# Kernel optimization log

Hardware: AMD Instinct MI355X
Metric: run time of the kernel (lower is better)

Reference implementation:

```python
import jax, jax.numpy as jnp
import numpy as np

A, NA, D_OBS, B = 16, 8, 64, 128  # agents, actions, obs dim, graphs
DZ = D_OBS + NA  # obs_z_input_dim = 72


def _mlp(x, W1, b1, W2, b2):
    # Linear -> leaky_relu(0.01) -> Linear, torch Linear convention (y = x @ W.T + b)
    return jax.nn.leaky_relu(x @ W1.T + b1) @ W2.T + b2


def setup_inputs() -> dict:
    key = jax.random.key(0)
    ks = iter(jax.random.split(key, 40))
    p = {}
    p["obs"] = jax.random.normal(next(ks), (B * A, D_OBS), jnp.float32)
    p["policies"] = jax.random.uniform(next(ks), (B * A, NA), jnp.float32)
    p["actions"] = jax.random.uniform(next(ks), (B * A, NA), jnp.float32)

    def mk(name, inp, out):
        p[name + "_w"] = jax.random.normal(next(ks), (out, inp), jnp.float32) / np.sqrt(inp).astype(np.float32)
        p[name + "_b"] = jax.random.normal(next(ks), (out,), jnp.float32) * 0.01

    mk("kw1", D_OBS, 64); mk("kw2", 64, 64)   # key_weight layers
    mk("qw1", D_OBS, 64); mk("qw2", 64, 64)   # query_weight layers
    mk("ko1", DZ, 64);    mk("ko2", 64, 64)   # key_obsz layers
    mk("qo1", DZ, 64);    mk("qo2", 64, 64)   # query_obsz layers
    mk("av1", DZ, 64);    mk("av2", 64, 64)   # attention_value_obsz layers
    mk("fv1", 128, 64);   mk("fv2", 64, 8)    # final_value layers
    return p


def reference(obs, policies, actions,
              kw1_w, kw1_b, kw2_w, kw2_b, qw1_w, qw1_b, qw2_w, qw2_b,
              ko1_w, ko1_b, ko2_w, ko2_b, qo1_w, qo1_b, qo2_w, qo2_b,
              av1_w, av1_b, av2_w, av2_b, fv1_w, fv1_b, fv2_w, fv2_b):
    d_k_w = jnp.sqrt(jnp.float32(kw2_w.shape[0]))
    d_k_o = jnp.sqrt(jnp.float32(ko2_w.shape[0]))
    Bn = obs.shape[0] // A
    obs_b = obs.reshape(Bn, A, -1)                      # [B,A,Dobs]
    pi = policies.reshape(Bn, A, NA)
    act = actions.reshape(Bn, A, NA)

    # --- DGL update_all on the fully-connected (with self-loop) per-batch graph ---
    key_z = _mlp(obs_b, kw1_w, kw1_b, kw2_w, kw2_b)     # [B,A,dk]
    query_z = _mlp(obs_b, qw1_w, qw1_b, qw2_w, qw2_b)
    score = jnp.einsum('bjd,bid->bij', key_z, query_z)  # src key j -> dst query i
    w = jax.nn.sigmoid(score / d_k_w)[..., None]        # [B,A,A,1], mailbox gate
    z = w * act[:, None] + (1.0 - w) * pi[:, None]      # [B,A(i),A(j),NA]
    weight_z = w.reshape(Bn * A, A, 1)

    # obs_z[b,i,j] = cat(obs[b,j], z[b,i,j])
    obs_rep = jnp.broadcast_to(obs_b[:, None], (Bn, A, A, obs_b.shape[-1]))
    obs_z = jnp.concatenate([obs_rep, z], axis=-1)      # [B,A,A,DZ]

    diag = jnp.arange(A)
    src = obs_z[:, diag, diag]                          # source_obs_z_: [B,A,DZ] (j==i entry)

    key_o = _mlp(src, ko1_w, ko1_b, ko2_w, ko2_b)       # broadcast over j
    query_o = _mlp(obs_z, qo1_w, qo1_b, qo2_w, qo2_b)   # [B,A,A,dk]
    score_o = jnp.einsum('bid,bijd->bij', key_o, query_o)
    weights_o = jax.nn.softmax(jnp.exp(jnp.clip(score_o / d_k_o, -5.0, 5.0)), axis=-1)  # [B,A,A]

    # obs_z_pi[b,i,j,k] = op[b,j] if k==j else obs_z[b,i,k], op = cat(obs, pi)
    op = jnp.concatenate([obs_b, pi], axis=-1)          # [B,A,DZ]
    m = jnp.eye(A, dtype=obs.dtype)[None, None, :, :, None]          # (j,k) mask
    obs_z_pi = obs_z[:, :, None] * (1.0 - m) + op[:, None, None] * m  # [B,A,A,A,DZ]

    attn_src = _mlp(src, av1_w, av1_b, av2_w, av2_b)                  # [B,A,O]
    attn_other = _mlp(obs_z_pi, av1_w, av1_b, av2_w, av2_b)           # [B,A,A,A,O]

    w_exp = weights_o[:, None, :, :, None]              # [b,i,j,k,1] = weights_o[b,j,k]
    mixed = jnp.mean(attn_other * w_exp, axis=-2)       # mean over k -> [B,A,A,O]
    src_rep = jnp.broadcast_to(attn_src[:, None], mixed.shape)
    node_features = jnp.concatenate([src_rep, mixed], axis=-1)        # [B,A,A,2O]
    value = _mlp(node_features, fv1_w, fv1_b, fv2_w, fv2_b)           # [B,A,A,8]

    weights_obsz = jnp.broadcast_to(w_exp, (Bn, A, A, A, 1))
    return value, weight_z, weights_obsz
```

## Files before the change

kernel.cpp:

```cpp
#include <hip/hip_runtime.h>

#define A_ 16
#define NA_ 8
#define DOBS_ 64

typedef _Float16 f16;
typedef f16 h2 __attribute__((ext_vector_type(2)));
typedef f16 v8h __attribute__((ext_vector_type(8)));
typedef float v4f __attribute__((ext_vector_type(4)));

__device__ __forceinline__ float fdot2f(h2 a, h2 b, float c) {
  return __builtin_amdgcn_fdot2(a, b, c, false);
}
__device__ __forceinline__ float lrelu(float x) { return x > 0.f ? x : 0.01f * x; }

struct P {
  const float *obs, *pol, *act;
  const float *kw1w, *kw1b, *kw2w, *kw2b, *qw1w, *qw1b, *qw2w, *qw2b;
  const float *ko1w, *ko1b, *ko2w, *ko2b, *qo1w, *qo1b, *qo2w, *qo2b;
  const float *av1w, *av1b, *av2w, *av2b, *fv1w, *fv1b, *fv2w, *fv2b;
  float *out0, *out1, *out2;
};

#define OBSH 0
#define OBSL 1152
#define X1Ho 2304
#define X1Lo 3456
#define X2Ho 4608
#define X2Lo 5760
#define EHO  6912
#define FLT  7168
#define F_PI   0
#define F_ACT  128
#define F_WSIG 256
#define F_WO   512
#define F_C0   768
#define F_S2   784
#define F_S3G  1872
#define F_WZK  2960
#define F_WZQ  3472
#define F_B    3984
#define WKW1  15648
#define WQW1  20256
#define WKW2  24864
#define WQW2  29472
#define WKO1H 34080
#define WKO1L 38688
#define WKO2H 43296
#define WKO2L 47904
#define WQO1H 52512
#define WQO1L 57120
#define WQO2H 61728
#define WQO2L 66336
#define AV1H  15648
#define AV2H  21792
#define BACKB1 26400
#define SLA   26656
#define SLB   70944
#define AOSRC 77088
#define APTO  78240
#define FV1H  34080
#define FV2PW 42784
#define BACKB2 43296
#define LDS_F16 79776

__device__ __forceinline__ v4f gemm_plain(const f16* Xh, const f16* W, float bv, int nt, int lane) {
  const int m = lane & 15, q = lane >> 4;
  v4f acc = {bv, bv, bv, bv};
  const v8h a0 = *(const v8h*)(Xh + m * 72 + q * 8);
  const v8h a1 = *(const v8h*)(Xh + m * 72 + 32 + q * 8);
  const f16* wr = W + (nt * 16 + m) * 72 + q * 8;
  acc = __builtin_amdgcn_mfma_f32_16x16x32_f16(a0, *(const v8h*)wr, acc, 0, 0, 0);
  acc = __builtin_amdgcn_mfma_f32_16x16x32_f16(a1, *(const v8h*)(wr + 32), acc, 0, 0, 0);
  return acc;
}

__device__ __forceinline__ v4f gemm_tile(const f16* Xh, const f16* Xl,
                                         const f16* Wh, const f16* Wl,
                                         float bv, int nt, int lane) {
  const int m = lane & 15, q = lane >> 4;
  v4f acc = {bv, bv, bv, bv};
  const v8h ah0 = *(const v8h*)(Xh + m * 72 + q * 8);
  const v8h ah1 = *(const v8h*)(Xh + m * 72 + 32 + q * 8);
  const v8h al0 = *(const v8h*)(Xl + m * 72 + q * 8);
  const v8h al1 = *(const v8h*)(Xl + m * 72 + 32 + q * 8);
  const f16* wr = Wh + (nt * 16 + m) * 72 + q * 8;
  const v8h bh0 = *(const v8h*)(wr);
  const v8h bh1 = *(const v8h*)(wr + 32);
  const f16* wr2 = Wl + (nt * 16 + m) * 72 + q * 8;
  const v8h bl0 = *(const v8h*)(wr2);
  const v8h bl1 = *(const v8h*)(wr2 + 32);
  acc = __builtin_amdgcn_mfma_f32_16x16x32_f16(ah0, bh0, acc, 0, 0, 0);
  acc = __builtin_amdgcn_mfma_f32_16x16x32_f16(ah1, bh1, acc, 0, 0, 0);
  acc = __builtin_amdgcn_mfma_f32_16x16x32_f16(ah0, bl0, acc, 0, 0, 0);
  acc = __builtin_amdgcn_mfma_f32_16x16x32_f16(ah1, bl1, acc, 0, 0, 0);
  acc = __builtin_amdgcn_mfma_f32_16x16x32_f16(al0, bh0, acc, 0, 0, 0);
  acc = __builtin_amdgcn_mfma_f32_16x16x32_f16(al1, bh1, acc, 0, 0, 0);
  return acc;
}

__device__ __forceinline__ void writeX(f16* Xh, f16* Xl, v4f acc, int nt, int lane, bool relu) {
  const int m = lane & 15, q = lane >> 4;
#pragma unroll
  for (int reg = 0; reg < 4; reg++) {
    float y = acc[reg];
    if (relu) y = lrelu(y);
    const f16 yh = (f16)y;
    Xh[(q * 4 + reg) * 72 + nt * 16 + m] = yh;
    Xl[(q * 4 + reg) * 72 + nt * 16 + m] = (f16)(y - (float)yh);
  }
}

__device__ __forceinline__ void putP(f16* W, float4 v, int o, int rq) {
  h2* d = (h2*)(W + o * 72 + 4 * rq);
  d[0] = h2{(f16)v.x, (f16)v.y};
  d[1] = h2{(f16)v.z, (f16)v.w};
}

__device__ __forceinline__ void putW(f16* Wh, f16* Wl, float4 v, int o, int rq) {
  h2* dh = (h2*)(Wh + o * 72 + 4 * rq);
  h2* dl = (h2*)(Wl + o * 72 + 4 * rq);
  const f16 hx = (f16)v.x, hy = (f16)v.y, hz = (f16)v.z, hw = (f16)v.w;
  dh[0] = h2{hx, hy};
  dh[1] = h2{hz, hw};
  dl[0] = h2{(f16)(v.x - (float)hx), (f16)(v.y - (float)hy)};
  dl[1] = h2{(f16)(v.z - (float)hz), (f16)(v.w - (float)hw)};
}

__device__ __forceinline__ v8h bfrag(const f16* Wm, int stride, int nt, int ks, int lane) {
  const int n = lane & 15, q = lane >> 4;
  return *(const v8h*)(Wm + (nt * 16 + n) * stride + ks * 32 + q * 8);
}

__device__ __forceinline__ void av_mlp2(const f16* obsh, const f16* av1H, const f16* av2H,
                                        const float* av1b, const float* av2b,
                                        f16* Hbuf, v8h az, int lane, v4f acc2[4]) {
  const int m = lane & 15, q = lane >> 4;
  const v8h a0 = *(const v8h*)(obsh + m * 72 + q * 8);
  const v8h a1 = *(const v8h*)(obsh + m * 72 + 32 + q * 8);
#pragma unroll
  for (int nt = 0; nt < 4; nt++) {
    const float bv = av1b[nt * 16 + m];
    v4f acc = {bv, bv, bv, bv};
    acc = __builtin_amdgcn_mfma_f32_16x16x32_f16(a0, bfrag(av1H, 96, nt, 0, lane), acc, 0, 0, 0);
    acc = __builtin_amdgcn_mfma_f32_16x16x32_f16(a1, bfrag(av1H, 96, nt, 1, lane), acc, 0, 0, 0);
    acc = __builtin_amdgcn_mfma_f32_16x16x32_f16(az, bfrag(av1H, 96, nt, 2, lane), acc, 0, 0, 0);
#pragma unroll
    for (int reg = 0; reg < 4; reg++)
      Hbuf[(q * 4 + reg) * 72 + nt * 16 + m] = (f16)lrelu(acc[reg]);
  }
  const v8h h0 = *(const v8h*)(Hbuf + m * 72 + q * 8);
  const v8h h1 = *(const v8h*)(Hbuf + m * 72 + 32 + q * 8);
#pragma unroll
  for (int nt = 0; nt < 4; nt++) {
    const float bv = av2b[nt * 16 + m];
    v4f acc = {bv, bv, bv, bv};
    acc = __builtin_amdgcn_mfma_f32_16x16x32_f16(h0, bfrag(av2H, 72, nt, 0, lane), acc, 0, 0, 0);
    acc = __builtin_amdgcn_mfma_f32_16x16x32_f16(h1, bfrag(av2H, 72, nt, 1, lane), acc, 0, 0, 0);
    acc2[nt] = acc;
  }
}

__global__ __launch_bounds__(512) void critic_fused(P p) {
  extern __shared__ f16 SMB[];
  float* F = (float*)(SMB + FLT);
  const int tid = threadIdx.x;
  const int b = blockIdx.x >> 1, ihalf = blockIdx.x & 1;
  const int w = tid >> 6, lane = tid & 63;
  const int m = lane & 15, quad = lane >> 4;
  const int o = tid & 63, r8 = tid >> 6;

  const float2 Robs = ((const float2*)(p.obs + (size_t)b * 1024))[tid];
  float Rpa = 0.f;
  if (tid < 128) Rpa = p.pol[(size_t)b * 128 + tid];
  else if (tid < 256) Rpa = p.act[(size_t)b * 128 + tid - 128];
  const float Rwzko = p.ko1w[(tid >> 3) * 72 + 64 + (tid & 7)];
  const float Rwzqo = p.qo1w[(tid >> 3) * 72 + 64 + (tid & 7)];
  float4 Rkw1[2], Rqw1[2], Rkw2[2], Rqw2[2], Rko1[2], Rko2[2], Rqo1[2], Rqo2[2];
#pragma unroll
  for (int h = 0; h < 2; h++) {
    const int rq = r8 + 8 * h;
    Rkw1[h] = *(const float4*)(p.kw1w + o * 64 + 4 * rq);
    Rqw1[h] = *(const float4*)(p.qw1w + o * 64 + 4 * rq);
    Rkw2[h] = *(const float4*)(p.kw2w + o * 64 + 4 * rq);
    Rqw2[h] = *(const float4*)(p.qw2w + o * 64 + 4 * rq);
    Rko1[h] = *(const float4*)(p.ko1w + o * 72 + 4 * rq);
    Rko2[h] = *(const float4*)(p.ko2w + o * 64 + 4 * rq);
    Rqo1[h] = *(const float4*)(p.qo1w + o * 72 + 4 * rq);
    Rqo2[h].x = p.qo2w[(4 * rq + 0) * 64 + o];
    Rqo2[h].y = p.qo2w[(4 * rq + 1) * 64 + o];
    Rqo2[h].z = p.qo2w[(4 * rq + 2) * 64 + o];
    Rqo2[h].w = p.qo2w[(4 * rq + 3) * 64 + o];
  }
  const int bi = (w & 3) * 16 + m;
  const float bias1 = (w < 4 ? p.kw1b : p.qw1b)[bi];
  const float bias2 = (w < 4 ? p.kw2b : p.qw2b)[bi];
  float rbo1 = 0.f, rbo2 = 0.f, rbo3 = 0.f, rbo4 = 0.f;
  if (tid < 64) { rbo1 = p.ko1b[tid]; rbo2 = p.ko2b[tid]; rbo3 = p.qo1b[tid]; rbo4 = p.qo2b[tid]; }
  const float4 rav1a = ((const float4*)p.av1w)[tid * 2];
  const float4 rav1b = ((const float4*)p.av1w)[tid * 2 + 1];
  const float rav1c = p.av1w[4096 + tid];
  const float4 rav2a = ((const float4*)p.av2w)[tid * 2];
  const float4 rav2b = ((const float4*)p.av2w)[tid * 2 + 1];
  float4 rfv[4];
#pragma unroll
  for (int qq = 0; qq < 4; qq++) rfv[qq] = ((const float4*)p.fv1w)[tid * 4 + qq];
  const float rfv2 = p.fv2w[tid];
  float rb1 = 0.f, rb2 = 0.f, rb3 = 0.f, rb4 = 0.f;
  if (tid < 64) { rb1 = p.av1b[tid]; rb2 = p.av2b[tid]; rb3 = p.fv1b[tid]; }
  if (tid < 8) rb4 = p.fv2b[tid];

  {
    const int e0 = 2 * tid, r0 = e0 >> 6, c0i = e0 & 63;
    const f16 hx = (f16)Robs.x, hy = (f16)Robs.y;
    *(h2*)(SMB + OBSH + r0 * 72 + c0i) = h2{hx, hy};
    *(h2*)(SMB + OBSL + r0 * 72 + c0i) = h2{(f16)(Robs.x - (float)hx), (f16)(Robs.y - (float)hy)};
  }
  if (tid < 128) F[F_PI + tid] = Rpa;
  else if (tid < 256) F[F_ACT + tid - 128] = Rpa;
  F[F_WZK + tid] = Rwzko;
  { const int oo = tid >> 3, c = tid & 7; F[F_WZQ + (oo & 15) * 32 + (oo >> 4) * 8 + c] = Rwzqo; }
  if (tid < 64) {
    F[F_B + tid] = rbo1; F[F_B + 64 + tid] = rbo2;
    F[F_B + 128 + tid] = rbo3; F[F_B + 192 + tid] = rbo4;
  }
#pragma unroll
  for (int h = 0; h < 2; h++) {
    const int rq = r8 + 8 * h;
    putP(SMB + WKW1, Rkw1[h], o, rq);
    putP(SMB + WQW1, Rqw1[h], o, rq);
    putP(SMB + WKW2, Rkw2[h], o, rq);
    putP(SMB + WQW2, Rqw2[h], o, rq);
    putW(SMB + WKO1H, SMB + WKO1L, Rko1[h], o, rq);
    putW(SMB + WKO2H, SMB + WKO2L, Rko2[h], o, rq);
    putW(SMB + WQO1H, SMB + WQO1L, Rqo1[h], o, rq);
    putW(SMB + WQO2H, SMB + WQO2L, Rqo2[h], o, rq);
  }
  __syncthreads();

  {
    const f16* Wp = (w < 4) ? (SMB + WKW1) : (SMB + WQW1);
    f16* Xo = (w < 4) ? (SMB + X1Ho) : (SMB + X2Ho);
    v4f a = gemm_plain(SMB + OBSH, Wp, bias1, w & 3, lane);
#pragma unroll
    for (int reg = 0; reg < 4; reg++)
      Xo[(quad * 4 + reg) * 72 + (w & 3) * 16 + m] = (f16)lrelu(a[reg]);
  }
  __syncthreads();

  {
    const f16* Wp = (w < 4) ? (SMB + WKW2) : (SMB + WQW2);
    const f16* Xi = (w < 4) ? (SMB + X1Ho) : (SMB + X2Ho);
    float* So = (w < 4) ? (F + F_S2) : (F + F_S3G);
    v4f a = gemm_plain(Xi, Wp, bias2, w & 3, lane);
#pragma unroll
    for (int reg = 0; reg < 4; reg++)
      So[(quad * 4 + reg) * 68 + (w & 3) * 16 + m] = a[reg];
  }
  __syncthreads();

  {
    const int idx = tid >> 1, g2 = tid & 1;
    const int i = idx >> 4, j = idx & 15;
    float a0 = 0.f, a1 = 0.f, a2 = 0.f, a3 = 0.f;
#pragma unroll
    for (int t4 = 0; t4 < 8; t4++) {
      const float4 qv = *(const float4*)(F + F_S3G + i * 68 + g2 * 32 + 4 * t4);
      const float4 kv = *(const float4*)(F + F_S2 + j * 68 + g2 * 32 + 4 * t4);
      a0 += qv.x * kv.x; a1 += qv.y * kv.y; a2 += qv.z * kv.z; a3 += qv.w * kv.w;
    }
    float sc = (a0 + a1) + (a2 + a3);
    sc += __shfl_xor(sc, 1);
    if (g2 == 0) {
      const float wv = 1.f / (1.f + __expf(-sc * 0.125f));
      F[F_WSIG + idx] = wv;
      p.out1[(size_t)b * 256 + idx] = wv;
    }
  }
  {
    float av1v[8] = {rav1a.x, rav1a.y, rav1a.z, rav1a.w, rav1b.x, rav1b.y, rav1b.z, rav1b.w};
#pragma unroll
    for (int e = 0; e < 8; e++) {
      const int k = tid * 8 + e, rr = k / 72, cc = k - rr * 72;
      SMB[AV1H + rr * 96 + cc] = (f16)av1v[e];
    }
    const int k = 4096 + tid, rr = k / 72, cc = k - rr * 72;
    SMB[AV1H + rr * 96 + cc] = (f16)rav1c;
    const int row = tid >> 3, c0p = 72 + (tid & 7) * 3;
#pragma unroll
    for (int c = 0; c < 3; c++) SMB[AV1H + row * 96 + c0p + c] = (f16)0.f;
    float av2v[8] = {rav2a.x, rav2a.y, rav2a.z, rav2a.w, rav2b.x, rav2b.y, rav2b.z, rav2b.w};
#pragma unroll
    for (int e = 0; e < 8; e++) {
      const int k2 = tid * 8 + e;
      SMB[AV2H + (k2 >> 6) * 72 + (k2 & 63)] = (f16)av2v[e];
    }
    float* BF1 = (float*)(SMB + BACKB1);
    if (tid < 64) { BF1[tid] = rb1; BF1[64 + tid] = rb2; }
  }
  __syncthreads();

  const float* BF1 = (const float*)(SMB + BACKB1);
  if (w == 0) {
#pragma unroll
    for (int nt = 0; nt < 4; nt++) {
      v4f a = gemm_tile(SMB + OBSH, SMB + OBSL, SMB + WKO1H, SMB + WKO1L, F[F_B + nt * 16 + m], nt, lane);
      const int oo = nt * 16 + m;
      float wzv[8];
      *(float4*)wzv = *(const float4*)(F + F_WZK + oo * 8);
      *(float4*)(wzv + 4) = *(const float4*)(F + F_WZK + oo * 8 + 4);
#pragma unroll
      for (int reg = 0; reg < 4; reg++) {
        const int rr = quad * 4 + reg;
        const float wrr = F[F_WSIG + rr * 17];
        float zp = 0.f;
#pragma unroll
        for (int c = 0; c < 8; c++) {
          const float zc = F[F_PI + rr * 8 + c] + wrr * (F[F_ACT + rr * 8 + c] - F[F_PI + rr * 8 + c]);
          zp += wzv[c] * zc;
        }
        const float y = lrelu(a[reg] + zp);
        const f16 yh = (f16)y;
        SMB[X2Ho + rr * 72 + oo] = yh;
        SMB[X2Lo + rr * 72 + oo] = (f16)(y - (float)yh);
      }
    }
#pragma unroll
    for (int nt = 0; nt < 4; nt++) {
      v4f a = gemm_tile(SMB + X2Ho, SMB + X2Lo, SMB + WKO2H, SMB + WKO2L, F[F_B + 64 + nt * 16 + m], nt, lane);
      writeX(SMB + X1Ho, SMB + X1Lo, a, nt, lane, false);
    }
#pragma unroll
    for (int nt = 0; nt < 4; nt++) {
      v4f a = gemm_tile(SMB + X1Ho, SMB + X1Lo, SMB + WQO2H, SMB + WQO2L, 0.f, nt, lane);
#pragma unroll
      for (int reg = 0; reg < 4; reg++)
        F[F_S2 + (quad * 4 + reg) * 68 + nt * 16 + m] = a[reg];
    }
    {
      const int r = lane >> 2, cs = (lane & 3) * 16;
      float t = 0.f;
#pragma unroll
      for (int c = 0; c < 16; c++) {
        const float kv = (float)SMB[X1Ho + r * 72 + cs + c] + (float)SMB[X1Lo + r * 72 + cs + c];
        t += kv * F[F_B + 192 + cs + c];
      }
      t += __shfl_xor(t, 1);
      t += __shfl_xor(t, 2);
      if ((lane & 3) == 0) F[F_C0 + r] = t;
    }
  } else if (w == 1) {
#pragma unroll
    for (int nt = 0; nt < 4; nt++) {
      v4f a = gemm_tile(SMB + OBSH, SMB + OBSL, SMB + WQO1H, SMB + WQO1L, F[F_B + 128 + nt * 16 + m], nt, lane);
#pragma unroll
      for (int reg = 0; reg < 4; reg++)
        F[F_S3G + m * 68 + (quad * 4 + reg) * 4 + nt] = a[reg];
    }
  } else {
    auto do_task = [&](int t) {
      f16* Hb;
      v8h az = {};
      if (t < 8) {
        Hb = (t < 4) ? (SMB + SLA + t * 1536) : (SMB + SLB + (t - 4) * 1536);
        if (quad == 0) {
          const float wv = F[F_WSIG + (ihalf * 8 + t) * 16 + m];
#pragma unroll
          for (int c = 0; c < 8; c++)
            az[c] = (f16)(F[F_PI + m * 8 + c] + wv * (F[F_ACT + m * 8 + c] - F[F_PI + m * 8 + c]));
        }
      } else if (t == 8) {
        Hb = SMB + APTO;
        if (quad == 0) {
#pragma unroll
          for (int c = 0; c < 8; c++) az[c] = (f16)F[F_PI + m * 8 + c];
        }
      } else {
        Hb = SMB + AOSRC;
        if (quad == 0) {
          const float wv = F[F_WSIG + m * 17];
#pragma unroll
          for (int c = 0; c < 8; c++)
            az[c] = (f16)(F[F_PI + m * 8 + c] + wv * (F[F_ACT + m * 8 + c] - F[F_PI + m * 8 + c]));
        }
      }
      v4f acc2[4];
      av_mlp2(SMB + OBSH, SMB + AV1H, SMB + AV2H, BF1, BF1 + 64, Hb, az, lane, acc2);
      if (t < 9) {
#pragma unroll
        for (int nt = 0; nt < 4; nt++)
#pragma unroll
          for (int reg = 0; reg < 4; reg++)
            Hb[(nt * 16 + m) * 24 + quad * 4 + reg] = (f16)acc2[nt][reg];
      } else {
#pragma unroll
        for (int nt = 0; nt < 4; nt++)
#pragma unroll
          for (int reg = 0; reg < 4; reg++)
            SMB[AOSRC + (quad * 4 + reg) * 72 + nt * 16 + m] = (f16)acc2[nt][reg];
      }
    };
    do_task(w - 2);
    if (w - 2 < 4) do_task(w - 2 + 6);
  }
  __syncthreads();

  {
    const int idx = tid >> 1, g2 = tid & 1;
    const int i = idx >> 4, j = idx & 15;
    const float wij = F[F_WSIG + i * 16 + j];
    float z[8];
#pragma unroll
    for (int c = 0; c < 8; c++)
      z[c] = F[F_PI + j * 8 + c] + wij * (F[F_ACT + j * 8 + c] - F[F_PI + j * 8 + c]);
    float sc = 0.f;
#pragma unroll
    for (int gg = 2 * g2; gg <= 2 * g2 + 1; gg++) {
#pragma unroll
      for (int t = 0; t < 16; t++) {
        const float4 wa = *(const float4*)(F + F_WZQ + t * 32 + gg * 8);
        const float4 wb = *(const float4*)(F + F_WZQ + t * 32 + gg * 8 + 4);
        float hv = F[F_S3G + t * 68 + j * 4 + gg]
          + wa.x * z[0] + wa.y * z[1] + wa.z * z[2] + wa.w * z[3]
          + wb.x * z[4] + wb.y * z[5] + wb.z * z[6] + wb.w * z[7];
        hv = lrelu(hv);
        sc += F[F_S2 + i * 68 + gg * 16 + t] * hv;
      }
    }
    sc += __shfl_xor(sc, 1);
    if (g2 == 0) {
      float yv = (sc + F[F_C0 + i]) * 0.125f;
      yv = fminf(fmaxf(yv, -5.f), 5.f);
      SMB[EHO + idx] = (f16)__expf(yv);
    }
  }
#pragma unroll
  for (int qq = 0; qq < 4; qq++) {
    const int e0 = tid * 16 + qq * 4;
    h2* d = (h2*)&SMB[FV1H + (e0 >> 7) * 136 + (e0 & 127)];
    d[0] = h2{(f16)rfv[qq].x, (f16)rfv[qq].y};
    d[1] = h2{(f16)rfv[qq].z, (f16)rfv[qq].w};
  }
  SMB[FV2PW + tid] = (f16)rfv2;
  {
    float* BF2 = (float*)(SMB + BACKB2);
    if (tid < 64) BF2[tid] = rb3;
    if (tid < 8) BF2[64 + tid] = rb4;
  }
  __syncthreads();

  if (tid < 256) {
    const int i = tid >> 4, j = tid & 15;
    float ev[16]; float mx = -1e30f;
#pragma unroll
    for (int jj = 0; jj < 16; jj++) { ev[jj] = (float)SMB[EHO + i * 16 + jj]; mx = fmaxf(mx, ev[jj]); }
    float den = 0.f;
#pragma unroll
    for (int jj = 0; jj < 16; jj++) den += __expf(ev[jj] - mx);
    F[F_WO + tid] = __expf(ev[j] - mx) / den;
  }
  __syncthreads();

  {
    const float* BF2 = (const float*)(SMB + BACKB2);
    const int i_ = ihalf * 8 + w;
    f16* Sl = (w < 4) ? (SMB + SLA + w * 1536) : (SMB + SLB + (w - 4) * 1536);
    v8h am;
#pragma unroll
    for (int e = 0; e < 8; e++) {
      const int j2 = quad * 8 + e;
      float v;
      if (j2 < 16) v = F[F_WO + m * 16 + j2] * 0.0625f;
      else v = (j2 - 16 == m) ? F[F_WO + m * 17] * 0.0625f : 0.f;
      am[e] = (f16)v;
    }
    {
      v4f macc[4];
#pragma unroll
      for (int nt = 0; nt < 4; nt++) {
        const int oo = nt * 16 + m;
        v8h bf;
        if (quad < 2) {
          bf = *(const v8h*)(Sl + oo * 24 + quad * 8);
        } else {
          const v8h apv = *(const v8h*)(&SMB[APTO + oo * 24 + (quad - 2) * 8]);
          const v8h aov = *(const v8h*)(Sl + oo * 24 + (quad - 2) * 8);
          bf = apv - aov;
        }
        v4f z4 = {0.f, 0.f, 0.f, 0.f};
        macc[nt] = __builtin_amdgcn_mfma_f32_16x16x32_f16(am, bf, z4, 0, 0, 0);
      }
#pragma unroll
      for (int nt = 0; nt < 4; nt++)
#pragma unroll
        for (int reg = 0; reg < 4; reg++)
          Sl[(quad * 4 + reg) * 72 + nt * 16 + m] = (f16)macc[nt][reg];
    }
    {
      const v8h f0 = *(const v8h*)(&SMB[AOSRC + m * 72 + quad * 8]);
      const v8h f1 = *(const v8h*)(&SMB[AOSRC + m * 72 + 32 + quad * 8]);
      const v8h f2 = *(const v8h*)(Sl + m * 72 + quad * 8);
      const v8h f3 = *(const v8h*)(Sl + m * 72 + 32 + quad * 8);
#pragma unroll
      for (int nt = 0; nt < 4; nt++) {
        const float bv = BF2[nt * 16 + m];
        v4f acc = {bv, bv, bv, bv};
        acc = __builtin_amdgcn_mfma_f32_16x16x32_f16(f0, bfrag(SMB + FV1H, 136, nt, 0, lane), acc, 0, 0, 0);
        acc = __builtin_amdgcn_mfma_f32_16x16x32_f16(f1, bfrag(SMB + FV1H, 136, nt, 1, lane), acc, 0, 0, 0);
        acc = __builtin_amdgcn_mfma_f32_16x16x32_f16(f2, bfrag(SMB + FV1H, 136, nt, 2, lane), acc, 0, 0, 0);
        acc = __builtin_amdgcn_mfma_f32_16x16x32_f16(f3, bfrag(SMB + FV1H, 136, nt, 3, lane), acc, 0, 0, 0);
#pragma unroll
        for (int reg = 0; reg < 4; reg++)
          Sl[(quad * 4 + reg) * 72 + nt * 16 + m] = (f16)lrelu(acc[reg]);
      }
    }
    {
      const int g2 = quad;
      float y0 = BF2[64 + 2 * g2], y1 = BF2[64 + 2 * g2 + 1];
#pragma unroll
      for (int o2 = 0; o2 < 32; o2++) {
        const h2 hh = *(const h2*)(Sl + m * 72 + 2 * o2);
        const h2 w0v = *(const h2*)(&SMB[FV2PW + (2 * g2) * 64 + 2 * o2]);
        const h2 w1v = *(const h2*)(&SMB[FV2PW + (2 * g2 + 1) * 64 + 2 * o2]);
        y0 = fdot2f(w0v, hh, y0);
        y1 = fdot2f(w1v, hh, y1);
      }
      *(float2*)(p.out0 + ((size_t)b * 256 + i_ * 16 + m) * 8 + 2 * g2) = make_float2(y0, y1);
    }
    {
      const float4 wv4 = *(const float4*)(F + F_WO + m * 16 + quad * 4);
      *(float4*)(p.out2 + ((size_t)b * 256 + i_ * 16 + m) * 16 + quad * 4) = wv4;
    }
  }
}

extern "C" void kernel_launch(void* const* d_in, const int* in_sizes, int n_in,
                              void* d_out, int out_size, void* d_ws, size_t ws_size,
                              hipStream_t stream) {
  P p;
  p.obs = (const float*)d_in[0];
  p.pol = (const float*)d_in[1];
  p.act = (const float*)d_in[2];
  p.kw1w = (const float*)d_in[3];  p.kw1b = (const float*)d_in[4];
  p.kw2w = (const float*)d_in[5];  p.kw2b = (const float*)d_in[6];
  p.qw1w = (const float*)d_in[7];  p.qw1b = (const float*)d_in[8];
  p.qw2w = (const float*)d_in[9];  p.qw2b = (const float*)d_in[10];
  p.ko1w = (const float*)d_in[11]; p.ko1b = (const float*)d_in[12];
  p.ko2w = (const float*)d_in[13]; p.ko2b = (const float*)d_in[14];
  p.qo1w = (const float*)d_in[15]; p.qo1b = (const float*)d_in[16];
  p.qo2w = (const float*)d_in[17]; p.qo2b = (const float*)d_in[18];
  p.av1w = (const float*)d_in[19]; p.av1b = (const float*)d_in[20];
  p.av2w = (const float*)d_in[21]; p.av2b = (const float*)d_in[22];
  p.fv1w = (const float*)d_in[23]; p.fv1b = (const float*)d_in[24];
  p.fv2w = (const float*)d_in[25]; p.fv2b = (const float*)d_in[26];

  const int Bn = in_sizes[0] / (A_ * DOBS_);
  p.out0 = (float*)d_out;
  p.out1 = p.out0 + (size_t)Bn * A_ * A_ * NA_;
  p.out2 = p.out1 + (size_t)Bn * A_ * A_;

  const size_t lds_bytes = (size_t)LDS_F16 * sizeof(f16);
  (void)hipFuncSetAttribute(reinterpret_cast<const void*>(critic_fused),
                            hipFuncAttributeMaxDynamicSharedMemorySize, (int)lds_bytes);
  hipLaunchKernelGGL(critic_fused, dim3(2 * Bn), dim3(512), lds_bytes, stream, p);
}
```

Baseline: 131.0 us.

## Rebalance per-wave work across phases to shorten the serial critical path

The ko/qo GEMM chain that wave 0 ran alone is now split across waves 0-1 (key path) and 2-3 (query path), each doing two column tiles. The av MLP tasks are redistributed over the remaining waves in two phases, with extra barriers between phases. The softmax is moved ahead of the FV weight staging so it shares a barrier with it. This cuts the longest single-wave chain at the cost of more block-wide synchronisation points.

```diff
diff --git a/kernel.cpp b/kernel.cpp
--- a/kernel.cpp
+++ b/kernel.cpp
@@ -295,15 +295,59 @@
       const int k2 = tid * 8 + e;
       SMB[AV2H + (k2 >> 6) * 72 + (k2 & 63)] = (f16)av2v[e];
     }
-    float* BF1 = (float*)(SMB + BACKB1);
-    if (tid < 64) { BF1[tid] = rb1; BF1[64 + tid] = rb2; }
+    float* BF1w = (float*)(SMB + BACKB1);
+    if (tid < 64) { BF1w[tid] = rb1; BF1w[64 + tid] = rb2; }
   }
   __syncthreads();
 
   const float* BF1 = (const float*)(SMB + BACKB1);
-  if (w == 0) {
-#pragma unroll
-    for (int nt = 0; nt < 4; nt++) {
+  auto do_av_task = [&](int t) {
+    f16* Hb;
+    v8h az = {};
+    if (t < 8) {
+      Hb = (t < 4) ? (SMB + SLA + t * 1536) : (SMB + SLB + (t - 4) * 1536);
+      if (quad == 0) {
+        const float wv = F[F_WSIG + (ihalf * 8 + t) * 16 + m];
+#pragma unroll
+        for (int c = 0; c < 8; c++)
+          az[c] = (f16)(F[F_PI + m * 8 + c] + wv * (F[F_ACT + m * 8 + c] - F[F_PI + m * 8 + c]));
+      }
+    } else if (t == 8) {
+      Hb = SMB + APTO;
+      if (quad == 0) {
+#pragma unroll
+        for (int c = 0; c < 8; c++) az[c] = (f16)F[F_PI + m * 8 + c];
+      }
+    } else {
+      Hb = SMB + AOSRC;
+      if (quad == 0) {
+        const float wv = F[F_WSIG + m * 17];
+#pragma unroll
+        for (int c = 0; c < 8; c++)
+          az[c] = (f16)(F[F_PI + m * 8 + c] + wv * (F[F_ACT + m * 8 + c] - F[F_PI + m * 8 + c]));
+      }
+    }
+    v4f acc2[4];
+    av_mlp2(SMB + OBSH, SMB + AV1H, SMB + AV2H, BF1, BF1 + 64, Hb, az, lane, acc2);
+    if (t < 9) {
+#pragma unroll
+      for (int nt = 0; nt < 4; nt++)
+#pragma unroll
+        for (int reg = 0; reg < 4; reg++)
+          Hb[(nt * 16 + m) * 24 + quad * 4 + reg] = (f16)acc2[nt][reg];
+    } else {
+#pragma unroll
+      for (int nt = 0; nt < 4; nt++)
+#pragma unroll
+        for (int reg = 0; reg < 4; reg++)
+          SMB[AOSRC + (quad * 4 + reg) * 72 + nt * 16 + m] = (f16)acc2[nt][reg];
+    }
+  };
+
+  if (w < 2) {
+#pragma unroll
+    for (int k2 = 0; k2 < 2; k2++) {
+      const int nt = w * 2 + k2;
       v4f a = gemm_tile(SMB + OBSH, SMB + OBSL, SMB + WKO1H, SMB + WKO1L, F[F_B + nt * 16 + m], nt, lane);
       const int oo = nt * 16 + m;
       float wzv[8];
@@ -325,83 +369,58 @@
         SMB[X2Lo + rr * 72 + oo] = (f16)(y - (float)yh);
       }
     }
-#pragma unroll
-    for (int nt = 0; nt < 4; nt++) {
+  } else if (w < 4) {
+#pragma unroll
+    for (int k2 = 0; k2 < 2; k2++) {
+      const int nt = (w - 2) * 2 + k2;
+      v4f a = gemm_tile(SMB + OBSH, SMB + OBSL, SMB + WQO1H, SMB + WQO1L, F[F_B + 128 + nt * 16 + m], nt, lane);
+#pragma unroll
+      for (int reg = 0; reg < 4; reg++)
+        F[F_S3G + m * 68 + (quad * 4 + reg) * 4 + nt] = a[reg];
+    }
+  } else {
+    do_av_task(w - 4);
+  }
+  __syncthreads();
+
+  if (w < 2) {
+#pragma unroll
+    for (int k2 = 0; k2 < 2; k2++) {
+      const int nt = w * 2 + k2;
       v4f a = gemm_tile(SMB + X2Ho, SMB + X2Lo, SMB + WKO2H, SMB + WKO2L, F[F_B + 64 + nt * 16 + m], nt, lane);
       writeX(SMB + X1Ho, SMB + X1Lo, a, nt, lane, false);
     }
-#pragma unroll
-    for (int nt = 0; nt < 4; nt++) {
+  } else if (w == 2) {
+    do_av_task(8);
+  } else if (w == 3) {
+    do_av_task(9);
+  } else {
+    do_av_task(w);
+  }
+  __syncthreads();
+
+  if (w < 2) {
+#pragma unroll
+    for (int k2 = 0; k2 < 2; k2++) {
+      const int nt = w * 2 + k2;
       v4f a = gemm_tile(SMB + X1Ho, SMB + X1Lo, SMB + WQO2H, SMB + WQO2L, 0.f, nt, lane);
 #pragma unroll
       for (int reg = 0; reg < 4; reg++)
         F[F_S2 + (quad * 4 + reg) * 68 + nt * 16 + m] = a[reg];
     }
     {
-      const int r = lane >> 2, cs = (lane & 3) * 16;
+      const int rr = tid >> 3, cs = (tid & 7) * 8;
       float t = 0.f;
 #pragma unroll
-      for (int c = 0; c < 16; c++) {
-        const float kv = (float)SMB[X1Ho + r * 72 + cs + c] + (float)SMB[X1Lo + r * 72 + cs + c];
+      for (int c = 0; c < 8; c++) {
+        const float kv = (float)SMB[X1Ho + rr * 72 + cs + c] + (float)SMB[X1Lo + rr * 72 + cs + c];
         t += kv * F[F_B + 192 + cs + c];
       }
       t += __shfl_xor(t, 1);
       t += __shfl_xor(t, 2);
-      if ((lane & 3) == 0) F[F_C0 + r] = t;
-    }
-  } else if (w == 1) {
-#pragma unroll
-    for (int nt = 0; nt < 4; nt++) {
-      v4f a = gemm_tile(SMB + OBSH, SMB + OBSL, SMB + WQO1H, SMB + WQO1L, F[F_B + 128 + nt * 16 + m], nt, lane);
-#pragma unroll
-      for (int reg = 0; reg < 4; reg++)
-        F[F_S3G + m * 68 + (quad * 4 + reg) * 4 + nt] = a[reg];
-    }
-  } else {
-    auto do_task = [&](int t) {
-      f16* Hb;
-      v8h az = {};
-      if (t < 8) {
-        Hb = (t < 4) ? (SMB + SLA + t * 1536) : (SMB + SLB + (t - 4) * 1536);
-        if (quad == 0) {
-          const float wv = F[F_WSIG + (ihalf * 8 + t) * 16 + m];
-#pragma unroll
-          for (int c = 0; c < 8; c++)
-            az[c] = (f16)(F[F_PI + m * 8 + c] + wv * (F[F_ACT + m * 8 + c] - F[F_PI + m * 8 + c]));
-        }
-      } else if (t == 8) {
-        Hb = SMB + APTO;
-        if (quad == 0) {
-#pragma unroll
-          for (int c = 0; c < 8; c++) az[c] = (f16)F[F_PI + m * 8 + c];
-        }
-      } else {
-        Hb = SMB + AOSRC;
-        if (quad == 0) {
-          const float wv = F[F_WSIG + m * 17];
-#pragma unroll
-          for (int c = 0; c < 8; c++)
-            az[c] = (f16)(F[F_PI + m * 8 + c] + wv * (F[F_ACT + m * 8 + c] - F[F_PI + m * 8 + c]));
-        }
-      }
-      v4f acc2[4];
-      av_mlp2(SMB + OBSH, SMB + AV1H, SMB + AV2H, BF1, BF1 + 64, Hb, az, lane, acc2);
-      if (t < 9) {
-#pragma unroll
-        for (int nt = 0; nt < 4; nt++)
-#pragma unroll
-          for (int reg = 0; reg < 4; reg++)
-            Hb[(nt * 16 + m) * 24 + quad * 4 + reg] = (f16)acc2[nt][reg];
-      } else {
-#pragma unroll
-        for (int nt = 0; nt < 4; nt++)
-#pragma unroll
-          for (int reg = 0; reg < 4; reg++)
-            SMB[AOSRC + (quad * 4 + reg) * 72 + nt * 16 + m] = (f16)acc2[nt][reg];
-      }
-    };
-    do_task(w - 2);
-    if (w - 2 < 4) do_task(w - 2 + 6);
+      t += __shfl_xor(t, 4);
+      if ((tid & 7) == 0) F[F_C0 + rr] = t;
+    }
   }
   __syncthreads();
 
@@ -434,6 +453,18 @@
       SMB[EHO + idx] = (f16)__expf(yv);
     }
   }
+  __syncthreads();
+
+  if (tid < 256) {
+    const int i = tid >> 4, j = tid & 15;
+    float ev[16]; float mx = -1e30f;
+#pragma unroll
+    for (int jj = 0; jj < 16; jj++) { ev[jj] = (float)SMB[EHO + i * 16 + jj]; mx = fmaxf(mx, ev[jj]); }
+    float den = 0.f;
+#pragma unroll
+    for (int jj = 0; jj < 16; jj++) den += __expf(ev[jj] - mx);
+    F[F_WO + tid] = __expf(ev[j] - mx) / den;
+  }
 #pragma unroll
   for (int qq = 0; qq < 4; qq++) {
     const int e0 = tid * 16 + qq * 4;
@@ -443,21 +474,9 @@
   }
   SMB[FV2PW + tid] = (f16)rfv2;
   {
-    float* BF2 = (float*)(SMB + BACKB2);
-    if (tid < 64) BF2[tid] = rb3;
-    if (tid < 8) BF2[64 + tid] = rb4;
-  }
-  __syncthreads();
-
-  if (tid < 256) {
-    const int i = tid >> 4, j = tid & 15;
-    float ev[16]; float mx = -1e30f;
-#pragma unroll
-    for (int jj = 0; jj < 16; jj++) { ev[jj] = (float)SMB[EHO + i * 16 + jj]; mx = fmaxf(mx, ev[jj]); }
-    float den = 0.f;
-#pragma unroll
-    for (int jj = 0; jj < 16; jj++) den += __expf(ev[jj] - mx);
-    F[F_WO + tid] = __expf(ev[j] - mx) / den;
+    float* BF2w = (float*)(SMB + BACKB2);
+    if (tid < 64) BF2w[tid] = rb3;
+    if (tid < 8) BF2w[64 + tid] = rb4;
   }
   __syncthreads();
 
```

Result: faster. 125.8 us (-4.0%).
